# Optimization experiments

Hardware: AMD Instinct MI355X
Metric: run time of the kernel (lower is better)

Reference implementation:

```python
import jax, jax.numpy as jnp
import numpy as np

B, CIN, T, H, W = 2, 256, 16, 16, 8
FF, COUT, NHEADS = 512, 256, 8
TEMP = 16.0
BN_EPS = 1e-5


def setup_inputs() -> dict:
    key = jax.random.key(0)
    ks = jax.random.split(key, 6)
    s_in = 1.0 / np.sqrt(CIN)
    s_ff = 1.0 / np.sqrt(FF)
    return {
        "x": jax.random.normal(ks[0], (B, CIN, T, H, W), jnp.float32),
        "WK": jax.random.uniform(ks[1], (FF, CIN), jnp.float32, -s_in, s_in),
        "WQ": jax.random.uniform(ks[2], (FF, CIN), jnp.float32, -s_in, s_in),
        "WV": jax.random.uniform(ks[3], (FF, CIN), jnp.float32, -s_in, s_in),
        "Wo": jax.random.uniform(ks[4], (COUT, FF), jnp.float32, -s_ff, s_ff),
        "bo": jax.random.uniform(ks[5], (COUT,), jnp.float32, -s_ff, s_ff),
        "gamma": jnp.ones((COUT,), jnp.float32),
        "beta": jnp.zeros((COUT,), jnp.float32),
    }


def reference(x, WK, WQ, WV, Wo, bo, gamma, beta):
    N = T * H * W
    xf = x.reshape(B, CIN, N)  # 1x1 conv3d == channel matmul
    dh = FF // NHEADS
    K = jnp.einsum("fc,bcn->bfn", WK, xf).reshape(B, NHEADS, dh, N)
    Q = jnp.einsum("fc,bcn->bfn", WQ, xf).reshape(B, NHEADS, dh, N)
    V = jnp.einsum("fc,bcn->bfn", WV, xf).reshape(B, NHEADS, dh, N)
    # KQ[b,h,i,j] = K_i . Q_j  (i = key token, j = query token, as in torch)
    KQ = jnp.einsum("bhdi,bhdj->bhij", K, Q) / TEMP
    # block-causal mask: token time index t = token_idx // (H*W); tril -> allow i >= j
    t_idx = jnp.arange(N) // (H * W)
    allow = t_idx[:, None] >= t_idx[None, :]  # (N, N)
    KQ = jnp.where(allow[None, None], KQ, -jnp.inf)
    attn = jax.nn.softmax(KQ, axis=3)  # softmax over j (last dim), as in torch
    # out[b,h,d,i] = sum_j V[b,h,d,j] * attn[b,h,i,j]
    Vo = jnp.einsum("bhdj,bhij->bhdi", V, attn).reshape(B, FF, N)
    y = jnp.einsum("of,bfn->bon", Wo, Vo) + bo[None, :, None]
    y = jax.nn.relu(y).reshape(B, COUT, T, H, W)
    out = x + y  # skip: out_dim == in_dim
    # BatchNorm3d (training-mode batch stats, biased var)
    mean = out.mean(axis=(0, 2, 3, 4), keepdims=True)
    var = out.var(axis=(0, 2, 3, 4), keepdims=True)
    norm = (out - mean) * jax.lax.rsqrt(var + BN_EPS)
    return norm * gamma[None, :, None, None, None] + beta[None, :, None, None, None]
```

## Files before the change

kernel.cpp:

```cpp
#include <hip/hip_runtime.h>
#include <math.h>

#define BB_   2
#define CIN_  256
#define NTOK_ 2048
#define FF_   512
#define COUT_ 256
#define NH_   8
#define DH_   64
#define HW_   128
#define BNEPS_ 1e-5f
#define SCALE_LOG2_ 0.09016844005556021f

typedef __attribute__((ext_vector_type(8))) short short8;
typedef __attribute__((ext_vector_type(4))) short bfx4;
typedef __attribute__((ext_vector_type(4))) float f32x4;

#if __has_builtin(__builtin_amdgcn_mfma_f32_16x16x16_bf16)
#define MFMA16(a, b, c) __builtin_amdgcn_mfma_f32_16x16x16_bf16(a, b, c, 0, 0, 0)
#else
#define MFMA16(a, b, c) __builtin_amdgcn_mfma_f32_16x16x16bf16_1k(a, b, c, 0, 0, 0)
#endif

__device__ inline unsigned short f2bf(float f) {
  union { float f; unsigned u; } v; v.f = f;
  unsigned r = (v.u + 0x7FFF + ((v.u >> 16) & 1)) >> 16;
  return (unsigned short)r;
}

__device__ __forceinline__ void dma16(const unsigned short* g, unsigned short* l) {
  __builtin_amdgcn_global_load_lds(
      (const __attribute__((address_space(1))) void*)g,
      (__attribute__((address_space(3))) void*)l, 16, 0, 0);
}

__global__ __launch_bounds__(256) void prep_kernel(
    const float* __restrict__ x, const float* __restrict__ WK,
    const float* __restrict__ WQ, const float* __restrict__ WV,
    const float* __restrict__ Wo, unsigned short* __restrict__ xT,
    unsigned short* __restrict__ Wkb, unsigned short* __restrict__ Wqb,
    unsigned short* __restrict__ Wvb, unsigned short* __restrict__ Wob) {
  __shared__ float T[64 * 65];
  const int tid = threadIdx.x;
  const int bid = blockIdx.x;
  if (bid < 256) {
    const int b = bid >> 7;
    const int rem = bid & 127;
    const int n0 = (rem >> 2) * 64;
    const int c0 = (rem & 3) * 64;
#pragma unroll
    for (int p = 0; p < 4; ++p) {
      const int idx = tid + 256 * p;
      const int row = idx >> 4, col = (idx & 15) * 4;
      const float4 v =
          *(const float4*)(x + (size_t)(b * CIN_ + c0 + row) * NTOK_ + n0 + col);
      T[row * 65 + col + 0] = v.x; T[row * 65 + col + 1] = v.y;
      T[row * 65 + col + 2] = v.z; T[row * 65 + col + 3] = v.w;
    }
    __syncthreads();
#pragma unroll
    for (int p = 0; p < 2; ++p) {
      const int idx = tid + 256 * p;
      const int nl = idx >> 3, c8 = (idx & 7) * 8;
      unsigned short u[8];
#pragma unroll
      for (int i = 0; i < 8; ++i) u[i] = f2bf(T[(c8 + i) * 65 + nl]);
      *(uint4*)(xT + ((size_t)(b * NTOK_ + n0 + nl)) * CIN_ + c0 + c8) =
          *(uint4*)u;
    }
  } else {
    const int t = bid - 256;
    const int which = t >> 5, blk = t & 31;
    const float* src = which == 0 ? WK : which == 1 ? WQ : which == 2 ? WV : Wo;
    unsigned short* dst = which == 0 ? Wkb : which == 1 ? Wqb : which == 2 ? Wvb : Wob;
    const int base = blk * 4096 + tid * 16;
#pragma unroll
    for (int p = 0; p < 4; ++p) {
      const float4 v = *(const float4*)(src + base + p * 4);
      ushort4 u;
      u.x = f2bf(v.x); u.y = f2bf(v.y); u.z = f2bf(v.z); u.w = f2bf(v.w);
      *(ushort4*)(dst + base + p * 4) = u;
    }
  }
}

__global__ __launch_bounds__(256, 3) void qkv_kernel(
    const unsigned short* __restrict__ xT, const unsigned short* __restrict__ Wkb,
    const unsigned short* __restrict__ Wqb, const unsigned short* __restrict__ Wvb,
    unsigned short* __restrict__ Kb, unsigned short* __restrict__ Qb,
    unsigned short* __restrict__ Vt) {
  __shared__ unsigned short Wsh[128 * 72];
  __shared__ unsigned short Xsh[64 * 72];
  const int tid = threadIdx.x;
  const int lane = tid & 63, w = tid >> 6;
  const int lx = lane & 15, q = lane >> 4;
  const int wm = w >> 1, wn = w & 1;
  const int n0 = blockIdx.x * 64;
  const int f0 = blockIdx.y * 128;
  const int b = blockIdx.z / 3, which = blockIdx.z % 3;
  const unsigned short* Wb = which == 0 ? Wkb : which == 1 ? Wqb : Wvb;

  const int srow = tid >> 3;
  const int soff = (tid & 7) * 8;
  const unsigned short* Wg = Wb + (size_t)(f0 + srow) * CIN_ + soff;
  const unsigned short* Xg = xT + ((size_t)(b * NTOK_ + n0 + srow)) * CIN_ + soff;

  uint4 wr[4], xr[2];
#pragma unroll
  for (int r = 0; r < 4; ++r) wr[r] = *(const uint4*)(Wg + (size_t)(32 * r) * CIN_);
#pragma unroll
  for (int r = 0; r < 2; ++r) xr[r] = *(const uint4*)(Xg + (size_t)(32 * r) * CIN_);

  f32x4 acc[4][2];
#pragma unroll
  for (int i = 0; i < 4; ++i)
#pragma unroll
    for (int j = 0; j < 2; ++j) acc[i][j] = (f32x4){0.f, 0.f, 0.f, 0.f};

  for (int kk = 0; kk < 4; ++kk) {
    __syncthreads();
#pragma unroll
    for (int r = 0; r < 4; ++r) *(uint4*)(Wsh + (srow + 32 * r) * 72 + soff) = wr[r];
#pragma unroll
    for (int r = 0; r < 2; ++r) *(uint4*)(Xsh + (srow + 32 * r) * 72 + soff) = xr[r];
    if (kk < 3) {
      const int c0 = (kk + 1) * 64;
#pragma unroll
      for (int r = 0; r < 4; ++r) wr[r] = *(const uint4*)(Wg + (size_t)(32 * r) * CIN_ + c0);
#pragma unroll
      for (int r = 0; r < 2; ++r) xr[r] = *(const uint4*)(Xg + (size_t)(32 * r) * CIN_ + c0);
    }
    __syncthreads();
    short8 xF[2][2];
#pragma unroll
    for (int i = 0; i < 2; ++i) {
      xF[i][0] = *(const short8*)(Xsh + (32 * wn + 16 * i + lx) * 72 + q * 8);
      xF[i][1] = *(const short8*)(Xsh + (32 * wn + 16 * i + lx) * 72 + 32 + q * 8);
    }
    if (which < 2) {
#pragma unroll
      for (int i = 0; i < 4; ++i) {
        const short8 w0 = *(const short8*)(Wsh + (64 * wm + 16 * i + lx) * 72 + q * 8);
        const short8 w1 = *(const short8*)(Wsh + (64 * wm + 16 * i + lx) * 72 + 32 + q * 8);
#pragma unroll
        for (int j = 0; j < 2; ++j) {
          acc[i][j] = __builtin_amdgcn_mfma_f32_16x16x32_bf16(w0, xF[j][0], acc[i][j], 0, 0, 0);
          acc[i][j] = __builtin_amdgcn_mfma_f32_16x16x32_bf16(w1, xF[j][1], acc[i][j], 0, 0, 0);
        }
      }
    } else {
#pragma unroll
      for (int jf = 0; jf < 4; ++jf) {
        const short8 w0 = *(const short8*)(Wsh + (64 * wm + 16 * jf + lx) * 72 + q * 8);
        const short8 w1 = *(const short8*)(Wsh + (64 * wm + 16 * jf + lx) * 72 + 32 + q * 8);
#pragma unroll
        for (int i = 0; i < 2; ++i) {
          acc[jf][i] = __builtin_amdgcn_mfma_f32_16x16x32_bf16(xF[i][0], w0, acc[jf][i], 0, 0, 0);
          acc[jf][i] = __builtin_amdgcn_mfma_f32_16x16x32_bf16(xF[i][1], w1, acc[jf][i], 0, 0, 0);
        }
      }
    }
  }

  const int h = (f0 >> 6) + wm;
  if (which < 2) {
    unsigned short* Y = (which == 0 ? Kb : Qb);
    const float sc = (which == 0) ? SCALE_LOG2_ : 1.0f;
#pragma unroll
    for (int i = 0; i < 4; ++i)
#pragma unroll
      for (int j = 0; j < 2; ++j) {
        const int n = n0 + 32 * wn + 16 * j + lx;
        const int d0 = 16 * i + 4 * q;
        ushort4 u;
        u.x = f2bf(acc[i][j][0] * sc); u.y = f2bf(acc[i][j][1] * sc);
        u.z = f2bf(acc[i][j][2] * sc); u.w = f2bf(acc[i][j][3] * sc);
        *(ushort4*)(Y + ((size_t)((b * NH_ + h) * NTOK_ + n)) * DH_ + d0) = u;
      }
  } else {
#pragma unroll
    for (int jf = 0; jf < 4; ++jf)
#pragma unroll
      for (int i = 0; i < 2; ++i) {
        const int d = 16 * jf + lx;
        const int n = n0 + 32 * wn + 16 * i + 4 * q;
        ushort4 u;
        u.x = f2bf(acc[jf][i][0]); u.y = f2bf(acc[jf][i][1]);
        u.z = f2bf(acc[jf][i][2]); u.w = f2bf(acc[jf][i][3]);
        *(ushort4*)(Vt + ((size_t)((b * NH_ + h) * DH_ + d)) * NTOK_ + n) = u;
      }
  }
}

__global__ __launch_bounds__(256, 2) void attn_kernel(
    const unsigned short* __restrict__ Kb, const unsigned short* __restrict__ Qb,
    const unsigned short* __restrict__ Vt, unsigned short* __restrict__ Ob) {
  __shared__ __align__(16) unsigned short Qbuf[2][8192];
  __shared__ __align__(16) unsigned short Vbuf[2][8192];

  const int tid = threadIdx.x;
  const int lane = tid & 63;
  const int w = tid >> 6;
  const int lx = lane & 15;
  const int g = lane >> 4;

  const int bid = blockIdx.x;
  const int xcd = bid & 7;
  const int k = bid >> 3;
  const int bh = xcd * 2 + (k & 1);
  const int u = k >> 1;
  const int iblk = (u < 16) ? (31 - u) : (u - 16);
  const int h = bh & 7, b = bh >> 3;
  const int i0 = iblk * 64;
  const int njt = (iblk >> 1) + 1;

  const size_t bhs = (size_t)b * NH_ + h;
  const unsigned short* Kg = Kb + bhs * (size_t)NTOK_ * DH_ + (size_t)i0 * DH_;
  const unsigned short* Qg = Qb + bhs * (size_t)NTOK_ * DH_;
  const unsigned short* Vg = Vt + bhs * (size_t)DH_ * NTOK_;

  auto stage = [&](int buf, int j0) {
#pragma unroll
    for (int cc = 0; cc < 4; ++cc) {
      const int chunk = 4 * w + cc;
      {
        const int row = chunk * 8 + (lane >> 3);
        const int grp = (lane & 7) ^ (row & 7);
        dma16(Qg + (size_t)(j0 + row) * DH_ + grp * 8, &Qbuf[buf][chunk * 512]);
      }
      {
        const int row = chunk * 4 + (lane >> 4);
        const int grp = (lane & 15) ^ (row & 7);
        dma16(Vg + (size_t)row * NTOK_ + j0 + grp * 8, &Vbuf[buf][chunk * 512]);
      }
    }
  };

  const short8 aK0 = *(const short8*)(Kg + (16 * w + lx) * DH_ + g * 8);
  const short8 aK1 = *(const short8*)(Kg + (16 * w + lx) * DH_ + 32 + g * 8);

  f32x4 o[4];
#pragma unroll
  for (int t = 0; t < 4; ++t) o[t] = (f32x4){0.f, 0.f, 0.f, 0.f};
  float rs = 0.f;

  const int fr0 = ((g ^ (lx & 7)) << 3);
  const int fr1 = (((4 + g) ^ (lx & 7)) << 3);

  stage(0, 0);
  __syncthreads();

  int cur = 0;
  for (int jt = 0; jt < njt; ++jt) {
    if (jt + 1 < njt) stage(cur ^ 1, (jt + 1) * 128);

    const unsigned short* Qs = Qbuf[cur];
    const unsigned short* Vs = Vbuf[cur];

    f32x4 sa[8];
#pragma unroll
    for (int s = 0; s < 8; ++s) {
      const int row = 16 * s + lx;
      const short8 a0 = *(const short8*)(Qs + row * 64 + fr0);
      const short8 a1 = *(const short8*)(Qs + row * 64 + fr1);
      sa[s] = (f32x4){0.f, 0.f, 0.f, 0.f};
      sa[s] = __builtin_amdgcn_mfma_f32_16x16x32_bf16(a0, aK0, sa[s], 0, 0, 0);
      sa[s] = __builtin_amdgcn_mfma_f32_16x16x32_bf16(a1, aK1, sa[s], 0, 0, 0);
    }

#pragma unroll
    for (int s = 0; s < 8; ++s) {
      const float p0 = __builtin_amdgcn_exp2f(sa[s][0]);
      const float p1 = __builtin_amdgcn_exp2f(sa[s][1]);
      const float p2 = __builtin_amdgcn_exp2f(sa[s][2]);
      const float p3 = __builtin_amdgcn_exp2f(sa[s][3]);
      rs += (p0 + p1) + (p2 + p3);
      union { unsigned u[2]; bfx4 v; } pk;
      pk.u[0] = (__builtin_bit_cast(unsigned, p0) >> 16) |
                (__builtin_bit_cast(unsigned, p1) & 0xFFFF0000u);
      pk.u[1] = (__builtin_bit_cast(unsigned, p2) >> 16) |
                (__builtin_bit_cast(unsigned, p3) & 0xFFFF0000u);
      const int jgrp = 2 * s + (g >> 1);
      const int joff = (g & 1) << 2;
#pragma unroll
      for (int t = 0; t < 4; ++t) {
        const int row = 16 * t + lx;
        const bfx4 va = *(const bfx4*)(Vs + row * 128 +
                                       ((jgrp ^ (row & 7)) << 3) + joff);
        o[t] = MFMA16(va, pk.v, o[t]);
      }
    }

    __syncthreads();
    cur ^= 1;
  }

  rs += __shfl_xor(rs, 16);
  rs += __shfl_xor(rs, 32);
  const float invl = 1.0f / rs;
  const int n = i0 + 16 * w + lx;
#pragma unroll
  for (int t = 0; t < 4; ++t) {
    ushort4 uo;
    uo.x = f2bf(o[t][0] * invl); uo.y = f2bf(o[t][1] * invl);
    uo.z = f2bf(o[t][2] * invl); uo.w = f2bf(o[t][3] * invl);
    *(ushort4*)(Ob + ((size_t)(b * NTOK_ + n)) * FF_ + h * 64 + 16 * t + 4 * g) = uo;
  }
}

__global__ __launch_bounds__(256) void proj_kernel(
    const unsigned short* __restrict__ Ob, const unsigned short* __restrict__ Wob,
    const float* __restrict__ bo, const float* __restrict__ x,
    float* __restrict__ pre) {
  __shared__ unsigned short Osh[64 * 72];
  __shared__ unsigned short Wsh[64 * 72];
  const int tid = threadIdx.x;
  const int lane = tid & 63, w = tid >> 6;
  const int lx = lane & 15, q = lane >> 4;
  const int wn = w & 1, wo = w >> 1;
  const int n0 = blockIdx.x * 64;
  const int o0 = blockIdx.y * 64;
  const int b = blockIdx.z;

  const int srow = tid >> 3;
  const int soff = (tid & 7) * 8;
  const unsigned short* Og = Ob + ((size_t)(b * NTOK_ + n0 + srow)) * FF_ + soff;
  const unsigned short* Wg = Wob + (size_t)(o0 + srow) * FF_ + soff;

  uint4 orr[2], wrr[2];
#pragma unroll
  for (int r = 0; r < 2; ++r) {
    orr[r] = *(const uint4*)(Og + (size_t)(32 * r) * FF_);
    wrr[r] = *(const uint4*)(Wg + (size_t)(32 * r) * FF_);
  }

  f32x4 acc[2][2];
#pragma unroll
  for (int i = 0; i < 2; ++i)
#pragma unroll
    for (int j = 0; j < 2; ++j) acc[i][j] = (f32x4){0.f, 0.f, 0.f, 0.f};

  for (int kk = 0; kk < 8; ++kk) {
    __syncthreads();
#pragma unroll
    for (int r = 0; r < 2; ++r) {
      *(uint4*)(Osh + (srow + 32 * r) * 72 + soff) = orr[r];
      *(uint4*)(Wsh + (srow + 32 * r) * 72 + soff) = wrr[r];
    }
    if (kk < 7) {
      const int c0 = (kk + 1) * 64;
#pragma unroll
      for (int r = 0; r < 2; ++r) {
        orr[r] = *(const uint4*)(Og + (size_t)(32 * r) * FF_ + c0);
        wrr[r] = *(const uint4*)(Wg + (size_t)(32 * r) * FF_ + c0);
      }
    }
    __syncthreads();
    short8 aF[2][2], bF[2][2];
#pragma unroll
    for (int i = 0; i < 2; ++i) {
      aF[i][0] = *(const short8*)(Osh + (32 * wn + 16 * i + lx) * 72 + q * 8);
      aF[i][1] = *(const short8*)(Osh + (32 * wn + 16 * i + lx) * 72 + 32 + q * 8);
      bF[i][0] = *(const short8*)(Wsh + (32 * wo + 16 * i + lx) * 72 + q * 8);
      bF[i][1] = *(const short8*)(Wsh + (32 * wo + 16 * i + lx) * 72 + 32 + q * 8);
    }
#pragma unroll
    for (int i = 0; i < 2; ++i)
#pragma unroll
      for (int j = 0; j < 2; ++j) {
        acc[i][j] = __builtin_amdgcn_mfma_f32_16x16x32_bf16(aF[i][0], bF[j][0], acc[i][j], 0, 0, 0);
        acc[i][j] = __builtin_amdgcn_mfma_f32_16x16x32_bf16(aF[i][1], bF[j][1], acc[i][j], 0, 0, 0);
      }
  }

#pragma unroll
  for (int j = 0; j < 2; ++j) {
    const int o = o0 + 32 * wo + 16 * j + lx;
    const float bias = bo[o];
#pragma unroll
    for (int i = 0; i < 2; ++i) {
      const int n = n0 + 32 * wn + 16 * i + 4 * q;
      const float4 xv = *(const float4*)(x + ((size_t)(b * CIN_ + o)) * NTOK_ + n);
      float4 v;
      v.x = fmaxf(acc[i][j][0] + bias, 0.f) + xv.x;
      v.y = fmaxf(acc[i][j][1] + bias, 0.f) + xv.y;
      v.z = fmaxf(acc[i][j][2] + bias, 0.f) + xv.z;
      v.w = fmaxf(acc[i][j][3] + bias, 0.f) + xv.w;
      *(float4*)(pre + ((size_t)(b * COUT_ + o)) * NTOK_ + n) = v;
    }
  }
}

__global__ __launch_bounds__(256) void bn_kernel(
    float* __restrict__ out, const float* __restrict__ gamma,
    const float* __restrict__ beta) {
  __shared__ float red[8];
  const int c = blockIdx.x;
  const int tid = threadIdx.x;
  const int lane = tid & 63, w = tid >> 6;

  float4 v[2][2];
  float s = 0.f, s2 = 0.f;
#pragma unroll
  for (int b = 0; b < BB_; ++b) {
    float* base = out + ((size_t)(b * COUT_ + c)) * NTOK_;
#pragma unroll
    for (int p = 0; p < 2; ++p) {
      const float4 t = *(const float4*)(base + 4 * tid + p * 1024);
      v[b][p] = t;
      s += t.x + t.y + t.z + t.w;
      s2 += t.x * t.x + t.y * t.y + t.z * t.z + t.w * t.w;
    }
  }
#pragma unroll
  for (int off = 32; off >= 1; off >>= 1) {
    s += __shfl_xor(s, off);
    s2 += __shfl_xor(s2, off);
  }
  if (lane == 0) { red[w] = s; red[4 + w] = s2; }
  __syncthreads();
  const float S = red[0] + red[1] + red[2] + red[3];
  const float S2 = red[4] + red[5] + red[6] + red[7];
  const float inv = 1.0f / (float)(BB_ * NTOK_);
  const float mean = S * inv;
  const float var = S2 * inv - mean * mean;
  const float sc = rsqrtf(var + BNEPS_) * gamma[c];
  const float bt = beta[c];
#pragma unroll
  for (int b = 0; b < BB_; ++b) {
    float* base = out + ((size_t)(b * COUT_ + c)) * NTOK_;
#pragma unroll
    for (int p = 0; p < 2; ++p) {
      float4 t = v[b][p];
      t.x = (t.x - mean) * sc + bt;
      t.y = (t.y - mean) * sc + bt;
      t.z = (t.z - mean) * sc + bt;
      t.w = (t.w - mean) * sc + bt;
      *(float4*)(base + 4 * tid + p * 1024) = t;
    }
  }
}

extern "C" void kernel_launch(void* const* d_in, const int* in_sizes, int n_in,
                              void* d_out, int out_size, void* d_ws, size_t ws_size,
                              hipStream_t stream) {
  (void)in_sizes; (void)n_in; (void)out_size; (void)ws_size;
  const float* x = (const float*)d_in[0];
  const float* WK = (const float*)d_in[1];
  const float* WQ = (const float*)d_in[2];
  const float* WV = (const float*)d_in[3];
  const float* Wo = (const float*)d_in[4];
  const float* bo = (const float*)d_in[5];
  const float* gamma = (const float*)d_in[6];
  const float* beta = (const float*)d_in[7];

  char* ws = (char*)d_ws;
  unsigned short* xT  = (unsigned short*)(ws);
  unsigned short* Wkb = (unsigned short*)(ws + 2097152);
  unsigned short* Wqb = (unsigned short*)(ws + 2359296);
  unsigned short* Wvb = (unsigned short*)(ws + 2621440);
  unsigned short* Wob = (unsigned short*)(ws + 2883584);
  unsigned short* Kb  = (unsigned short*)(ws + 3145728);
  unsigned short* Qb  = (unsigned short*)(ws + 7340032);
  unsigned short* Vt  = (unsigned short*)(ws + 11534336);
  unsigned short* Ob  = (unsigned short*)(ws + 15728640);
  float* out = (float*)d_out;

  prep_kernel<<<384, 256, 0, stream>>>(x, WK, WQ, WV, Wo, xT, Wkb, Wqb, Wvb, Wob);
  qkv_kernel<<<dim3(32, 4, 6), 256, 0, stream>>>(xT, Wkb, Wqb, Wvb, Kb, Qb, Vt);
  attn_kernel<<<dim3(512, 1, 1), 256, 0, stream>>>(Kb, Qb, Vt, Ob);
  proj_kernel<<<dim3(32, 4, 2), 256, 0, stream>>>(Ob, Wob, bo, x, out);
  bn_kernel<<<256, 256, 0, stream>>>(out, gamma, beta);
}
```

Baseline: 141.2 us.

## Fuse all stages into one persistent kernel with atomic grid barriers

Replaces the five separate kernel launches with a single 512-block persistent kernel that runs prep, QKV, attention, projection and batchnorm as stages separated by atomic-counter grid barriers, with a shared-memory union across stages. This aims to remove per-launch overhead and inter-kernel gaps. It relies on all 512 blocks being co-resident, adds barrier spin cost, forces one register budget across all stages, and leaves uneven qkv work distribution.

```diff
diff --git a/kernel.cpp b/kernel.cpp
--- a/kernel.cpp
+++ b/kernel.cpp
@@ -34,18 +34,40 @@
       (__attribute__((address_space(3))) void*)l, 16, 0, 0);
 }
 
-__global__ __launch_bounds__(256) void prep_kernel(
-    const float* __restrict__ x, const float* __restrict__ WK,
+union __align__(16) SmemU {
+  float prepT[64 * 65];
+  struct { unsigned short W[128 * 72]; unsigned short X[64 * 72]; } qkv;
+  struct { unsigned short Q[2][8192]; unsigned short V[2][8192]; } attn;
+  struct { unsigned short O[64 * 72]; unsigned short W[64 * 72]; } proj;
+  float red[8];
+};
+
+#define NBLK_ 512u
+
+__device__ __forceinline__ void gridbar(unsigned* ctr) {
+  __syncthreads();
+  if (threadIdx.x == 0) {
+    __hip_atomic_fetch_add(ctr, 1u, __ATOMIC_ACQ_REL, __HIP_MEMORY_SCOPE_AGENT);
+    while (__hip_atomic_load(ctr, __ATOMIC_ACQUIRE, __HIP_MEMORY_SCOPE_AGENT) <
+           NBLK_) {
+      __builtin_amdgcn_s_sleep(2);
+    }
+  }
+  __syncthreads();
+}
+
+__device__ __forceinline__ void prep_stage(
+    int vb, const float* __restrict__ x, const float* __restrict__ WK,
     const float* __restrict__ WQ, const float* __restrict__ WV,
     const float* __restrict__ Wo, unsigned short* __restrict__ xT,
     unsigned short* __restrict__ Wkb, unsigned short* __restrict__ Wqb,
-    unsigned short* __restrict__ Wvb, unsigned short* __restrict__ Wob) {
-  __shared__ float T[64 * 65];
+    unsigned short* __restrict__ Wvb, unsigned short* __restrict__ Wob,
+    SmemU& sm) {
   const int tid = threadIdx.x;
-  const int bid = blockIdx.x;
-  if (bid < 256) {
-    const int b = bid >> 7;
-    const int rem = bid & 127;
+  if (vb < 256) {
+    float* T = sm.prepT;
+    const int b = vb >> 7;
+    const int rem = vb & 127;
     const int n0 = (rem >> 2) * 64;
     const int c0 = (rem & 3) * 64;
 #pragma unroll
@@ -69,7 +91,7 @@
           *(uint4*)u;
     }
   } else {
-    const int t = bid - 256;
+    const int t = vb - 256;
     const int which = t >> 5, blk = t & 31;
     const float* src = which == 0 ? WK : which == 1 ? WQ : which == 2 ? WV : Wo;
     unsigned short* dst = which == 0 ? Wkb : which == 1 ? Wqb : which == 2 ? Wvb : Wob;
@@ -84,20 +106,22 @@
   }
 }
 
-__global__ __launch_bounds__(256, 3) void qkv_kernel(
-    const unsigned short* __restrict__ xT, const unsigned short* __restrict__ Wkb,
-    const unsigned short* __restrict__ Wqb, const unsigned short* __restrict__ Wvb,
-    unsigned short* __restrict__ Kb, unsigned short* __restrict__ Qb,
-    unsigned short* __restrict__ Vt) {
-  __shared__ unsigned short Wsh[128 * 72];
-  __shared__ unsigned short Xsh[64 * 72];
+__device__ __forceinline__ void qkv_stage(
+    int vb, const unsigned short* __restrict__ xT,
+    const unsigned short* __restrict__ Wkb, const unsigned short* __restrict__ Wqb,
+    const unsigned short* __restrict__ Wvb, unsigned short* __restrict__ Kb,
+    unsigned short* __restrict__ Qb, unsigned short* __restrict__ Vt,
+    SmemU& sm) {
+  unsigned short* Wsh = sm.qkv.W;
+  unsigned short* Xsh = sm.qkv.X;
   const int tid = threadIdx.x;
   const int lane = tid & 63, w = tid >> 6;
   const int lx = lane & 15, q = lane >> 4;
   const int wm = w >> 1, wn = w & 1;
-  const int n0 = blockIdx.x * 64;
-  const int f0 = blockIdx.y * 128;
-  const int b = blockIdx.z / 3, which = blockIdx.z % 3;
+  const int n0 = (vb & 31) * 64;
+  const int f0 = ((vb >> 5) & 3) * 128;
+  const int bz = vb >> 7;
+  const int b = bz / 3, which = bz % 3;
   const unsigned short* Wb = which == 0 ? Wkb : which == 1 ? Wqb : Wvb;
 
   const int srow = tid >> 3;
@@ -192,21 +216,18 @@
   }
 }
 
-__global__ __launch_bounds__(256, 2) void attn_kernel(
-    const unsigned short* __restrict__ Kb, const unsigned short* __restrict__ Qb,
-    const unsigned short* __restrict__ Vt, unsigned short* __restrict__ Ob) {
-  __shared__ __align__(16) unsigned short Qbuf[2][8192];
-  __shared__ __align__(16) unsigned short Vbuf[2][8192];
-
+__device__ __forceinline__ void attn_stage(
+    int vb, const unsigned short* __restrict__ Kb,
+    const unsigned short* __restrict__ Qb, const unsigned short* __restrict__ Vt,
+    unsigned short* __restrict__ Ob, SmemU& sm) {
   const int tid = threadIdx.x;
   const int lane = tid & 63;
   const int w = tid >> 6;
   const int lx = lane & 15;
   const int g = lane >> 4;
 
-  const int bid = blockIdx.x;
-  const int xcd = bid & 7;
-  const int k = bid >> 3;
+  const int xcd = vb & 7;
+  const int k = vb >> 3;
   const int bh = xcd * 2 + (k & 1);
   const int u = k >> 1;
   const int iblk = (u < 16) ? (31 - u) : (u - 16);
@@ -226,12 +247,12 @@
       {
         const int row = chunk * 8 + (lane >> 3);
         const int grp = (lane & 7) ^ (row & 7);
-        dma16(Qg + (size_t)(j0 + row) * DH_ + grp * 8, &Qbuf[buf][chunk * 512]);
+        dma16(Qg + (size_t)(j0 + row) * DH_ + grp * 8, &sm.attn.Q[buf][chunk * 512]);
       }
       {
         const int row = chunk * 4 + (lane >> 4);
         const int grp = (lane & 15) ^ (row & 7);
-        dma16(Vg + (size_t)row * NTOK_ + j0 + grp * 8, &Vbuf[buf][chunk * 512]);
+        dma16(Vg + (size_t)row * NTOK_ + j0 + grp * 8, &sm.attn.V[buf][chunk * 512]);
       }
     }
   };
@@ -254,8 +275,8 @@
   for (int jt = 0; jt < njt; ++jt) {
     if (jt + 1 < njt) stage(cur ^ 1, (jt + 1) * 128);
 
-    const unsigned short* Qs = Qbuf[cur];
-    const unsigned short* Vs = Vbuf[cur];
+    const unsigned short* Qs = sm.attn.Q[cur];
+    const unsigned short* Vs = sm.attn.V[cur];
 
     f32x4 sa[8];
 #pragma unroll
@@ -308,19 +329,19 @@
   }
 }
 
-__global__ __launch_bounds__(256) void proj_kernel(
-    const unsigned short* __restrict__ Ob, const unsigned short* __restrict__ Wob,
-    const float* __restrict__ bo, const float* __restrict__ x,
-    float* __restrict__ pre) {
-  __shared__ unsigned short Osh[64 * 72];
-  __shared__ unsigned short Wsh[64 * 72];
+__device__ __forceinline__ void proj_stage(
+    int vb, const unsigned short* __restrict__ Ob,
+    const unsigned short* __restrict__ Wob, const float* __restrict__ bo,
+    const float* __restrict__ x, float* __restrict__ pre, SmemU& sm) {
+  unsigned short* Osh = sm.proj.O;
+  unsigned short* Wsh = sm.proj.W;
   const int tid = threadIdx.x;
   const int lane = tid & 63, w = tid >> 6;
   const int lx = lane & 15, q = lane >> 4;
   const int wn = w & 1, wo = w >> 1;
-  const int n0 = blockIdx.x * 64;
-  const int o0 = blockIdx.y * 64;
-  const int b = blockIdx.z;
+  const int n0 = (vb & 31) * 64;
+  const int o0 = ((vb >> 5) & 3) * 64;
+  const int b = vb >> 7;
 
   const int srow = tid >> 3;
   const int soff = (tid & 7) * 8;
@@ -391,11 +412,10 @@
   }
 }
 
-__global__ __launch_bounds__(256) void bn_kernel(
-    float* __restrict__ out, const float* __restrict__ gamma,
-    const float* __restrict__ beta) {
-  __shared__ float red[8];
-  const int c = blockIdx.x;
+__device__ __forceinline__ void bn_stage(
+    int c, float* __restrict__ out, const float* __restrict__ gamma,
+    const float* __restrict__ beta, SmemU& sm) {
+  float* red = sm.red;
   const int tid = threadIdx.x;
   const int lane = tid & 63, w = tid >> 6;
 
@@ -439,6 +459,36 @@
       *(float4*)(base + 4 * tid + p * 1024) = t;
     }
   }
+}
+
+__global__ __launch_bounds__(256, 2) void mega_kernel(
+    const float* __restrict__ x, const float* __restrict__ WK,
+    const float* __restrict__ WQ, const float* __restrict__ WV,
+    const float* __restrict__ Wo, const float* __restrict__ bo,
+    const float* __restrict__ gamma, const float* __restrict__ beta,
+    unsigned short* __restrict__ xT, unsigned short* __restrict__ Wkb,
+    unsigned short* __restrict__ Wqb, unsigned short* __restrict__ Wvb,
+    unsigned short* __restrict__ Wob, unsigned short* __restrict__ Kb,
+    unsigned short* __restrict__ Qb, unsigned short* __restrict__ Vt,
+    unsigned short* __restrict__ Ob, float* __restrict__ out,
+    unsigned* bar) {
+  __shared__ SmemU sm;
+  const int gid = blockIdx.x;
+
+  if (gid < 384) prep_stage(gid, x, WK, WQ, WV, Wo, xT, Wkb, Wqb, Wvb, Wob, sm);
+  gridbar(bar + 0);
+
+  qkv_stage(gid, xT, Wkb, Wqb, Wvb, Kb, Qb, Vt, sm);
+  if (gid < 256) qkv_stage(gid + 512, xT, Wkb, Wqb, Wvb, Kb, Qb, Vt, sm);
+  gridbar(bar + 1);
+
+  attn_stage(gid, Kb, Qb, Vt, Ob, sm);
+  gridbar(bar + 2);
+
+  if (gid < 256) proj_stage(gid, Ob, Wob, bo, x, out, sm);
+  gridbar(bar + 3);
+
+  if (gid < 256) bn_stage(gid, out, gamma, beta, sm);
 }
 
 extern "C" void kernel_launch(void* const* d_in, const int* in_sizes, int n_in,
@@ -464,11 +514,11 @@
   unsigned short* Qb  = (unsigned short*)(ws + 7340032);
   unsigned short* Vt  = (unsigned short*)(ws + 11534336);
   unsigned short* Ob  = (unsigned short*)(ws + 15728640);
+  unsigned* bar = (unsigned*)(ws + 19922944);
   float* out = (float*)d_out;
 
-  prep_kernel<<<384, 256, 0, stream>>>(x, WK, WQ, WV, Wo, xT, Wkb, Wqb, Wvb, Wob);
-  qkv_kernel<<<dim3(32, 4, 6), 256, 0, stream>>>(xT, Wkb, Wqb, Wvb, Kb, Qb, Vt);
-  attn_kernel<<<dim3(512, 1, 1), 256, 0, stream>>>(Kb, Qb, Vt, Ob);
-  proj_kernel<<<dim3(32, 4, 2), 256, 0, stream>>>(Ob, Wob, bo, x, out);
-  bn_kernel<<<256, 256, 0, stream>>>(out, gamma, beta);
-}
+  hipMemsetAsync(bar, 0, 16, stream);
+  mega_kernel<<<512, 256, 0, stream>>>(x, WK, WQ, WV, Wo, bo, gamma, beta,
+                                       xT, Wkb, Wqb, Wvb, Wob, Kb, Qb, Vt, Ob,
+                                       out, bar);
+}
```

New measurement: 367.1 us. 2.6x slower.
